# Performance work log

Hardware: AMD Instinct MI355X
Metric: run time of the kernel (lower is better)

## Reference

```python
import jax, jax.numpy as jnp
import numpy as np
from jax import lax
from jax.scipy.special import logsumexp

NUM_TAGS = 5
B, L = 16384, 512


def setup_inputs() -> dict:
    key = jax.random.key(0)
    k1, k2, k3, k4, k5 = jax.random.split(key, 5)
    emissions = jax.random.normal(k1, (B, L, NUM_TAGS), dtype=jnp.float32)
    tags = jax.random.randint(k2, (B, L), 0, NUM_TAGS)
    mask = jnp.ones((B, L), dtype=bool)
    # learned CRF parameters, init U(-0.1, 0.1) as in reset_parameters
    transitions = jax.random.uniform(k3, (NUM_TAGS, NUM_TAGS), minval=-0.1, maxval=0.1, dtype=jnp.float32)
    start_transitions = jax.random.uniform(k4, (NUM_TAGS,), minval=-0.1, maxval=0.1, dtype=jnp.float32)
    end_transitions = jax.random.uniform(k5, (NUM_TAGS,), minval=-0.1, maxval=0.1, dtype=jnp.float32)
    return {
        "emissions": emissions,
        "transitions": transitions,
        "start_transitions": start_transitions,
        "end_transitions": end_transitions,
        "tags": tags,
        "mask": mask,
    }


def reference(emissions, transitions, start_transitions, end_transitions, tags, mask):
    """CRF mean negative log-likelihood: log_partition - gold_score (both batch means)."""
    Bs, Ls, C = emissions.shape
    maskf = mask.astype(emissions.dtype)

    # ---- log partition (forward algorithm); note: original torch code's
    # mask application here is a no-op (where(mask, s, s)), reproduced faithfully.
    init_score = start_transitions[None, :] + emissions[:, 0]  # (B, C)

    def step(score, em_i):
        # score: (B, C) over previous tag; em_i: (B, C)
        nxt = logsumexp(score[:, :, None] + transitions[None, :, :] + em_i[:, None, :], axis=1)
        return nxt, None

    ems = jnp.swapaxes(emissions[:, 1:], 0, 1)  # (L-1, B, C)
    final_score, _ = lax.scan(step, init_score, ems)
    log_den = logsumexp(final_score + end_transitions[None, :], axis=1).mean()

    # ---- gold path score (fully vectorized over time)
    s0 = start_transitions[tags[:, 0]] + jnp.take_along_axis(emissions[:, 0], tags[:, :1], axis=1)[:, 0]
    trans_scores = transitions[tags[:, :-1], tags[:, 1:]]  # (B, L-1)
    em_at_tags = jnp.take_along_axis(emissions, tags[:, :, None], axis=2)[:, :, 0]  # (B, L)
    path_score = s0 + ((trans_scores + em_at_tags[:, 1:]) * maskf[:, 1:]).sum(axis=1)
    last_idx = mask.sum(axis=1).astype(jnp.int32) - 1  # (B,)
    last_tags = jnp.take_along_axis(tags, last_idx[:, None], axis=1)[:, 0]
    log_num = (path_score + end_transitions[last_tags]).mean()

    return log_den - log_num
```

## Files before the change

kernel.cpp:

```cpp
#include <hip/hip_runtime.h>

#define NTAGS 5
#define BATCH 16384
#define SEQL 512
#define TT 4
#define RECF 32

__device__ __forceinline__ float f4c(float4 v, int c) {
    switch (c & 3) { case 0: return v.x; case 1: return v.y; case 2: return v.z; default: return v.w; }
}
__device__ __forceinline__ int i4c(int4 v, int c) {
    switch (c & 3) { case 0: return v.x; case 1: return v.y; case 2: return v.z; default: return v.w; }
}
__device__ __forceinline__ float sel5v(float a0, float a1, float a2, float a3, float a4, int t) {
    float r = a0;
    r = (t == 1) ? a1 : r;
    r = (t == 2) ? a2 : r;
    r = (t == 3) ? a3 : r;
    r = (t == 4) ? a4 : r;
    return r;
}
__device__ __forceinline__ float rfl(float x) {
    return __int_as_float(__builtin_amdgcn_readfirstlane(__float_as_int(x)));
}

struct P1State {
    float M[25];
    float logS;
    float path;
    int prev;
};

__device__ __forceinline__ void p1_tile(const float4 tb[5], const int4 tg, bool sk0,
                                        P1State& st, const float eT[25],
                                        const float* ldsT, const float stR[5]) {
#pragma unroll
    for (int t = 0; t < TT; ++t) {
#define EMX(j) f4c(tb[(t * 5 + (j)) >> 2], (t * 5 + (j)) & 3)
        const float e0 = EMX(0), e1 = EMX(1), e2 = EMX(2), e3 = EMX(3), e4 = EMX(4);
#undef EMX
        const int tag = i4c(tg, t);
        const float emtag = sel5v(e0, e1, e2, e3, e4, tag);
        if (sk0 && t == 0) {
            st.path += sel5v(stR[0], stR[1], stR[2], stR[3], stR[4], tag) + emtag;
        } else {
            const float ex0 = __expf(e0), ex1 = __expf(e1), ex2 = __expf(e2),
                        ex3 = __expf(e3), ex4 = __expf(e4);
#pragma unroll
            for (int i = 0; i < 5; ++i) {
                const float m0 = st.M[i * 5 + 0], m1 = st.M[i * 5 + 1], m2 = st.M[i * 5 + 2],
                            m3 = st.M[i * 5 + 3], m4 = st.M[i * 5 + 4];
#pragma unroll
                for (int j = 0; j < 5; ++j) {
                    float a = m0 * eT[j];
                    a = fmaf(m1, eT[5 + j], a);
                    a = fmaf(m2, eT[10 + j], a);
                    a = fmaf(m3, eT[15 + j], a);
                    a = fmaf(m4, eT[20 + j], a);
                    const float exj = (j == 0) ? ex0 : (j == 1) ? ex1 : (j == 2) ? ex2
                                     : (j == 3) ? ex3 : ex4;
                    st.M[i * 5 + j] = a * exj;
                }
            }
            st.path += ldsT[st.prev * 5 + tag] + emtag;
        }
        st.prev = tag;
    }
    float m = st.M[0];
#pragma unroll
    for (int i = 1; i < 25; ++i) m = fmaxf(m, st.M[i]);
    st.logS += __logf(m);
    const float rc = __builtin_amdgcn_rcpf(m);
#pragma unroll
    for (int i = 0; i < 25; ++i) st.M[i] *= rc;
}

template <int NCHUNK>
__global__ __launch_bounds__(256) void crf_phase1(
    const float* __restrict__ emis, const float* __restrict__ trans,
    const float* __restrict__ startT, const int* __restrict__ tags,
    float* __restrict__ ws) {
    constexpr int CHUNKL = SEQL / NCHUNK;
    constexpr int NTILE = CHUNKL / TT;
    __shared__ float ldsT[25];
    const int tid = threadIdx.x;
    if (tid < 25) ldsT[tid] = trans[tid];
    __syncthreads();

    float eT[25];
#pragma unroll
    for (int i = 0; i < 25; ++i) eT[i] = rfl(__expf(trans[i]));
    float stR[5];
#pragma unroll
    for (int j = 0; j < 5; ++j) stR[j] = rfl(startT[j]);

    const int gt = blockIdx.x * 256 + tid;
    const int seq = gt / NCHUNK;
    const int chunk = gt & (NCHUNK - 1);
    const bool first = (chunk == 0);

    const float4* esrc =
        (const float4*)(emis + (size_t)seq * (SEQL * NTAGS) + chunk * (CHUNKL * NTAGS));
    const int tbase = seq * SEQL + chunk * CHUNKL;
    const int4* tsrc = (const int4*)(tags + tbase);

    P1State st;
#pragma unroll
    for (int i = 0; i < 25; ++i) st.M[i] = 0.f;
    st.M[0] = st.M[6] = st.M[12] = st.M[18] = st.M[24] = 1.f;
    st.logS = 0.f;
    st.path = 0.f;
    st.prev = first ? 0 : tags[tbase - 1];

#pragma unroll 1
    for (int tp = 0; tp < NTILE; ++tp) {
        float4 tb[5];
#pragma unroll
        for (int k = 0; k < 5; ++k) tb[k] = esrc[tp * 5 + k];
        const int4 tg = tsrc[tp];
        p1_tile(tb, tg, first && (tp == 0), st, eT, ldsT, stR);
    }

    float4* rec = (float4*)(ws + (size_t)gt * RECF);
#pragma unroll
    for (int k = 0; k < 6; ++k)
        rec[k] = make_float4(st.M[4 * k], st.M[4 * k + 1], st.M[4 * k + 2], st.M[4 * k + 3]);
    rec[6] = make_float4(st.M[24], st.logS, st.path, 0.f);
}

__device__ __forceinline__ void p2_combine(const float4 r[7], float v[5], float& logZ,
                                           float& path) {
#define MM(i, j) f4c(r[((i) * 5 + (j)) >> 2], ((i) * 5 + (j)) & 3)
    float nv[5];
#pragma unroll
    for (int j = 0; j < 5; ++j) {
        float a = v[0] * MM(0, j);
        a = fmaf(v[1], MM(1, j), a);
        a = fmaf(v[2], MM(2, j), a);
        a = fmaf(v[3], MM(3, j), a);
        a = fmaf(v[4], MM(4, j), a);
        nv[j] = a;
    }
#undef MM
    logZ += r[6].y;
    path += r[6].z;
    const float m = fmaxf(fmaxf(fmaxf(nv[0], nv[1]), fmaxf(nv[2], nv[3])), nv[4]);
    logZ += __logf(m);
    const float rc = __builtin_amdgcn_rcpf(m);
#pragma unroll
    for (int j = 0; j < 5; ++j) v[j] = nv[j] * rc;
}

template <int NCHUNK>
__global__ __launch_bounds__(64) void crf_phase2(
    const float* __restrict__ emis, const float* __restrict__ startT,
    const float* __restrict__ endT, const int* __restrict__ tags,
    const float* __restrict__ ws, float* __restrict__ out) {
    const int seq = blockIdx.x * 64 + threadIdx.x;
    const float* eb = emis + (size_t)seq * (SEQL * NTAGS);
    const float4 e03 = *(const float4*)eb;
    const float e4v = eb[4];
    const float s0 = startT[0] + e03.x, s1 = startT[1] + e03.y, s2 = startT[2] + e03.z,
                s3 = startT[3] + e03.w, s4 = startT[4] + e4v;
    const float m0 = fmaxf(fmaxf(fmaxf(s0, s1), fmaxf(s2, s3)), s4);
    float v[5] = {__expf(s0 - m0), __expf(s1 - m0), __expf(s2 - m0), __expf(s3 - m0),
                  __expf(s4 - m0)};
    float logZ = m0, path = 0.f;

    const float4* wsb = (const float4*)(ws + (size_t)seq * NCHUNK * RECF);
    float4 rA[7], rB[7];
#pragma unroll
    for (int k = 0; k < 7; ++k) rA[k] = wsb[k];

#pragma unroll 1
    for (int c = 0; c < NCHUNK; c += 2) {
#pragma unroll
        for (int k = 0; k < 7; ++k) rB[k] = wsb[(c + 1) * 8 + k];
        p2_combine(rA, v, logZ, path);
        const int nx = (c + 2 < NCHUNK) ? c + 2 : c;
#pragma unroll
        for (int k = 0; k < 7; ++k) rA[k] = wsb[nx * 8 + k];
        p2_combine(rB, v, logZ, path);
    }

    const float en0 = endT[0], en1 = endT[1], en2 = endT[2], en3 = endT[3], en4 = endT[4];
    float sden = v[0] * __expf(en0);
    sden = fmaf(v[1], __expf(en1), sden);
    sden = fmaf(v[2], __expf(en2), sden);
    sden = fmaf(v[3], __expf(en3), sden);
    sden = fmaf(v[4], __expf(en4), sden);
    const float den = logZ + __logf(sden);

    const int lastTag = tags[seq * SEQL + (SEQL - 1)];
    const float num = path + sel5v(en0, en1, en2, en3, en4, lastTag);

    float val = (den - num) * (1.0f / (float)BATCH);
#pragma unroll
    for (int off = 32; off > 0; off >>= 1) val += __shfl_xor(val, off, 64);
    if (threadIdx.x == 0) atomicAdd(out, val);
}

extern "C" void kernel_launch(void* const* d_in, const int* in_sizes, int n_in,
                              void* d_out, int out_size, void* d_ws, size_t ws_size,
                              hipStream_t stream) {
    const float* emis = (const float*)d_in[0];
    const float* trans = (const float*)d_in[1];
    const float* startT = (const float*)d_in[2];
    const float* endT = (const float*)d_in[3];
    const int* tags = (const int*)d_in[4];
    float* out = (float*)d_out;
    float* ws = (float*)d_ws;

    hipMemsetAsync(out, 0, sizeof(float), stream);
    const size_t need16 = (size_t)BATCH * 16 * RECF * sizeof(float);
    if (ws_size >= need16) {
        crf_phase1<16><<<dim3(BATCH * 16 / 256), dim3(256), 0, stream>>>(emis, trans,
                                                                         startT, tags, ws);
        crf_phase2<16><<<dim3(BATCH / 64), dim3(64), 0, stream>>>(emis, startT, endT,
                                                                  tags, ws, out);
    } else {
        crf_phase1<8><<<dim3(BATCH * 8 / 256), dim3(256), 0, stream>>>(emis, trans,
                                                                       startT, tags, ws);
        crf_phase2<8><<<dim3(BATCH / 64), dim3(64), 0, stream>>>(emis, startT, endT,
                                                                 tags, ws, out);
    }
}
```

Measured before the change: 329.4 us.

## Stage emissions through LDS as bf16, use 32 chunks, pack bf16 chunk records

Phase 1 now uses 64-thread blocks that cooperatively load a contiguous emission and tag slab with coalesced float4 loads. The data goes into LDS, emissions as bf16 pairs and tags as bytes. Each thread then processes a 16-step chunk (32 chunks per sequence) with renormalization every 8 steps. Chunk matrices are written as bf16 in a transposed, batch-major layout so phase 2 reads them coalesced with half the bytes. This targets global-load inefficiency and workspace traffic, but rounding emissions and the transfer matrices to bf16 changes the numerics relative to fp32.

```diff
diff --git a/kernel.cpp b/kernel.cpp
--- a/kernel.cpp
+++ b/kernel.cpp
@@ -3,15 +3,11 @@
 #define NTAGS 5
 #define BATCH 16384
 #define SEQL 512
-#define TT 4
-#define RECF 32
-
-__device__ __forceinline__ float f4c(float4 v, int c) {
-    switch (c & 3) { case 0: return v.x; case 1: return v.y; case 2: return v.z; default: return v.w; }
-}
-__device__ __forceinline__ int i4c(int4 v, int c) {
-    switch (c & 3) { case 0: return v.x; case 1: return v.y; case 2: return v.z; default: return v.w; }
-}
+#define NCHUNK 32
+#define CHUNKL 16
+#define EW 41
+#define TW 5
+
 __device__ __forceinline__ float sel5v(float a0, float a1, float a2, float a3, float a4, int t) {
     float r = a0;
     r = (t == 1) ? a1 : r;
@@ -23,68 +19,45 @@
 __device__ __forceinline__ float rfl(float x) {
     return __int_as_float(__builtin_amdgcn_readfirstlane(__float_as_int(x)));
 }
-
-struct P1State {
-    float M[25];
-    float logS;
-    float path;
-    int prev;
-};
-
-__device__ __forceinline__ void p1_tile(const float4 tb[5], const int4 tg, bool sk0,
-                                        P1State& st, const float eT[25],
-                                        const float* ldsT, const float stR[5]) {
-#pragma unroll
-    for (int t = 0; t < TT; ++t) {
-#define EMX(j) f4c(tb[(t * 5 + (j)) >> 2], (t * 5 + (j)) & 3)
-        const float e0 = EMX(0), e1 = EMX(1), e2 = EMX(2), e3 = EMX(3), e4 = EMX(4);
-#undef EMX
-        const int tag = i4c(tg, t);
-        const float emtag = sel5v(e0, e1, e2, e3, e4, tag);
-        if (sk0 && t == 0) {
-            st.path += sel5v(stR[0], stR[1], stR[2], stR[3], stR[4], tag) + emtag;
-        } else {
-            const float ex0 = __expf(e0), ex1 = __expf(e1), ex2 = __expf(e2),
-                        ex3 = __expf(e3), ex4 = __expf(e4);
-#pragma unroll
-            for (int i = 0; i < 5; ++i) {
-                const float m0 = st.M[i * 5 + 0], m1 = st.M[i * 5 + 1], m2 = st.M[i * 5 + 2],
-                            m3 = st.M[i * 5 + 3], m4 = st.M[i * 5 + 4];
-#pragma unroll
-                for (int j = 0; j < 5; ++j) {
-                    float a = m0 * eT[j];
-                    a = fmaf(m1, eT[5 + j], a);
-                    a = fmaf(m2, eT[10 + j], a);
-                    a = fmaf(m3, eT[15 + j], a);
-                    a = fmaf(m4, eT[20 + j], a);
-                    const float exj = (j == 0) ? ex0 : (j == 1) ? ex1 : (j == 2) ? ex2
-                                     : (j == 3) ? ex3 : ex4;
-                    st.M[i * 5 + j] = a * exj;
-                }
-            }
-            st.path += ldsT[st.prev * 5 + tag] + emtag;
-        }
-        st.prev = tag;
-    }
-    float m = st.M[0];
-#pragma unroll
-    for (int i = 1; i < 25; ++i) m = fmaxf(m, st.M[i]);
-    st.logS += __logf(m);
-    const float rc = __builtin_amdgcn_rcpf(m);
-#pragma unroll
-    for (int i = 0; i < 25; ++i) st.M[i] *= rc;
-}
-
-template <int NCHUNK>
-__global__ __launch_bounds__(256) void crf_phase1(
+__device__ __forceinline__ unsigned bf16rne(float x) {
+    const unsigned b = __float_as_uint(x);
+    return (b + 0x7FFFu + ((b >> 16) & 1u)) >> 16;
+}
+__device__ __forceinline__ float bflo(unsigned w) { return __uint_as_float(w << 16); }
+__device__ __forceinline__ float bfhi(unsigned w) { return __uint_as_float(w & 0xFFFF0000u); }
+
+__global__ __launch_bounds__(64) void crf_phase1(
     const float* __restrict__ emis, const float* __restrict__ trans,
     const float* __restrict__ startT, const int* __restrict__ tags,
-    float* __restrict__ ws) {
-    constexpr int CHUNKL = SEQL / NCHUNK;
-    constexpr int NTILE = CHUNKL / TT;
+    int4* __restrict__ ws) {
+    __shared__ unsigned eLds[64 * EW];
+    __shared__ unsigned tagLds[64 * TW];
     __shared__ float ldsT[25];
+
     const int tid = threadIdx.x;
+    const int gt0 = blockIdx.x * 64;
     if (tid < 25) ldsT[tid] = trans[tid];
+
+    const float4* esrc4 = (const float4*)emis + (size_t)gt0 * 20;
+#pragma unroll
+    for (int i = 0; i < 20; ++i) {
+        const float4 v = esrc4[i * 64 + tid];
+        const int f = i * 256 + tid * 4;
+        const int tau = f / 80;
+        const int h = f - tau * 80;
+        eLds[tau * EW + (h >> 1)] = bf16rne(v.x) | (bf16rne(v.y) << 16);
+        eLds[tau * EW + (h >> 1) + 1] = bf16rne(v.z) | (bf16rne(v.w) << 16);
+    }
+    const int4* tsrc4 = (const int4*)tags + (size_t)gt0 * 4;
+#pragma unroll
+    for (int i = 0; i < 4; ++i) {
+        const int4 tv = tsrc4[i * 64 + tid];
+        const int g = i * 256 + tid * 4;
+        const int tau = g >> 4;
+        const int k = (g & 15) >> 2;
+        tagLds[tau * TW + k] = (unsigned)tv.x | ((unsigned)tv.y << 8) |
+                               ((unsigned)tv.z << 16) | ((unsigned)tv.w << 24);
+    }
     __syncthreads();
 
     float eT[25];
@@ -94,56 +67,113 @@
 #pragma unroll
     for (int j = 0; j < 5; ++j) stR[j] = rfl(startT[j]);
 
-    const int gt = blockIdx.x * 256 + tid;
-    const int seq = gt / NCHUNK;
-    const int chunk = gt & (NCHUNK - 1);
-    const bool first = (chunk == 0);
-
-    const float4* esrc =
-        (const float4*)(emis + (size_t)seq * (SEQL * NTAGS) + chunk * (CHUNKL * NTAGS));
-    const int tbase = seq * SEQL + chunk * CHUNKL;
-    const int4* tsrc = (const int4*)(tags + tbase);
-
-    P1State st;
-#pragma unroll
-    for (int i = 0; i < 25; ++i) st.M[i] = 0.f;
-    st.M[0] = st.M[6] = st.M[12] = st.M[18] = st.M[24] = 1.f;
-    st.logS = 0.f;
-    st.path = 0.f;
-    st.prev = first ? 0 : tags[tbase - 1];
-
-#pragma unroll 1
-    for (int tp = 0; tp < NTILE; ++tp) {
-        float4 tb[5];
-#pragma unroll
-        for (int k = 0; k < 5; ++k) tb[k] = esrc[tp * 5 + k];
-        const int4 tg = tsrc[tp];
-        p1_tile(tb, tg, first && (tp == 0), st, eT, ldsT, stR);
-    }
-
-    float4* rec = (float4*)(ws + (size_t)gt * RECF);
-#pragma unroll
-    for (int k = 0; k < 6; ++k)
-        rec[k] = make_float4(st.M[4 * k], st.M[4 * k + 1], st.M[4 * k + 2], st.M[4 * k + 3]);
-    rec[6] = make_float4(st.M[24], st.logS, st.path, 0.f);
-}
-
-__device__ __forceinline__ void p2_combine(const float4 r[7], float v[5], float& logZ,
+    float M[25];
+#pragma unroll
+    for (int i = 0; i < 25; ++i) M[i] = 0.f;
+    M[0] = M[6] = M[12] = M[18] = M[24] = 1.f;
+    float logS = 0.f, path = 0.f;
+    const bool first = (tid & 31) == 0;
+    int prev = first ? 0 : (int)(tagLds[(tid - 1) * TW + 3] >> 24);
+
+    const unsigned* eb = &eLds[tid * EW];
+    const unsigned* tb = &tagLds[tid * TW];
+
+#pragma unroll 2
+    for (int sp = 0; sp < 8; ++sp) {
+        const unsigned w0 = eb[sp * 5 + 0], w1 = eb[sp * 5 + 1], w2 = eb[sp * 5 + 2],
+                       w3 = eb[sp * 5 + 3], w4 = eb[sp * 5 + 4];
+        const unsigned twrd = tb[sp >> 1];
+#pragma unroll
+        for (int half = 0; half < 2; ++half) {
+            const int s = sp * 2 + half;
+            const float e0 = half ? bfhi(w2) : bflo(w0);
+            const float e1 = half ? bflo(w3) : bfhi(w0);
+            const float e2 = half ? bfhi(w3) : bflo(w1);
+            const float e3 = half ? bflo(w4) : bfhi(w1);
+            const float e4 = half ? bfhi(w4) : bflo(w2);
+            const int tag = (int)((twrd >> ((s & 3) * 8)) & 255u);
+            const float emtag = sel5v(e0, e1, e2, e3, e4, tag);
+            if (first && s == 0) {
+                path += sel5v(stR[0], stR[1], stR[2], stR[3], stR[4], tag) + emtag;
+            } else {
+                const float ex0 = __expf(e0), ex1 = __expf(e1), ex2 = __expf(e2),
+                            ex3 = __expf(e3), ex4 = __expf(e4);
+#pragma unroll
+                for (int i = 0; i < 5; ++i) {
+                    const float m0 = M[i * 5 + 0], m1 = M[i * 5 + 1], m2 = M[i * 5 + 2],
+                                m3 = M[i * 5 + 3], m4 = M[i * 5 + 4];
+#pragma unroll
+                    for (int j = 0; j < 5; ++j) {
+                        float a = m0 * eT[j];
+                        a = fmaf(m1, eT[5 + j], a);
+                        a = fmaf(m2, eT[10 + j], a);
+                        a = fmaf(m3, eT[15 + j], a);
+                        a = fmaf(m4, eT[20 + j], a);
+                        const float exj = (j == 0) ? ex0 : (j == 1) ? ex1 : (j == 2) ? ex2
+                                         : (j == 3) ? ex3 : ex4;
+                        M[i * 5 + j] = a * exj;
+                    }
+                }
+                path += ldsT[prev * 5 + tag] + emtag;
+            }
+            prev = tag;
+        }
+        if ((sp & 3) == 3) {
+            float m = M[0];
+#pragma unroll
+            for (int i = 1; i < 25; ++i) m = fmaxf(m, M[i]);
+            logS += __logf(m);
+            const float rc = __builtin_amdgcn_rcpf(m);
+#pragma unroll
+            for (int i = 0; i < 25; ++i) M[i] *= rc;
+        }
+    }
+
+    unsigned rw[16];
+#pragma unroll
+    for (int j = 0; j < 12; ++j) rw[j] = bf16rne(M[2 * j]) | (bf16rne(M[2 * j + 1]) << 16);
+    rw[12] = bf16rne(M[24]);
+    rw[13] = __float_as_uint(logS);
+    rw[14] = __float_as_uint(path);
+    rw[15] = 0u;
+    const int gt = gt0 + tid;
+    const int seq = gt >> 5, chunk = gt & 31;
+#pragma unroll
+    for (int k = 0; k < 4; ++k)
+        ws[(size_t)(chunk * 4 + k) * BATCH + seq] =
+            make_int4((int)rw[4 * k], (int)rw[4 * k + 1], (int)rw[4 * k + 2],
+                      (int)rw[4 * k + 3]);
+}
+
+__device__ __forceinline__ void p2_combine(const int4 r[4], float v[5], float& logZ,
                                            float& path) {
-#define MM(i, j) f4c(r[((i) * 5 + (j)) >> 2], ((i) * 5 + (j)) & 3)
+    unsigned w[16];
+#pragma unroll
+    for (int k = 0; k < 4; ++k) {
+        w[4 * k + 0] = (unsigned)r[k].x;
+        w[4 * k + 1] = (unsigned)r[k].y;
+        w[4 * k + 2] = (unsigned)r[k].z;
+        w[4 * k + 3] = (unsigned)r[k].w;
+    }
+    float M[25];
+#pragma unroll
+    for (int j = 0; j < 12; ++j) {
+        M[2 * j] = bflo(w[j]);
+        M[2 * j + 1] = bfhi(w[j]);
+    }
+    M[24] = bflo(w[12]);
     float nv[5];
 #pragma unroll
     for (int j = 0; j < 5; ++j) {
-        float a = v[0] * MM(0, j);
-        a = fmaf(v[1], MM(1, j), a);
-        a = fmaf(v[2], MM(2, j), a);
-        a = fmaf(v[3], MM(3, j), a);
-        a = fmaf(v[4], MM(4, j), a);
+        float a = v[0] * M[j];
+        a = fmaf(v[1], M[5 + j], a);
+        a = fmaf(v[2], M[10 + j], a);
+        a = fmaf(v[3], M[15 + j], a);
+        a = fmaf(v[4], M[20 + j], a);
         nv[j] = a;
     }
-#undef MM
-    logZ += r[6].y;
-    path += r[6].z;
+    logZ += __uint_as_float(w[13]);
+    path += __uint_as_float(w[14]);
     const float m = fmaxf(fmaxf(fmaxf(nv[0], nv[1]), fmaxf(nv[2], nv[3])), nv[4]);
     logZ += __logf(m);
     const float rc = __builtin_amdgcn_rcpf(m);
@@ -151,15 +181,14 @@
     for (int j = 0; j < 5; ++j) v[j] = nv[j] * rc;
 }
 
-template <int NCHUNK>
 __global__ __launch_bounds__(64) void crf_phase2(
     const float* __restrict__ emis, const float* __restrict__ startT,
     const float* __restrict__ endT, const int* __restrict__ tags,
-    const float* __restrict__ ws, float* __restrict__ out) {
+    const int4* __restrict__ ws, float* __restrict__ out) {
     const int seq = blockIdx.x * 64 + threadIdx.x;
-    const float* eb = emis + (size_t)seq * (SEQL * NTAGS);
-    const float4 e03 = *(const float4*)eb;
-    const float e4v = eb[4];
+    const float* ebp = emis + (size_t)seq * (SEQL * NTAGS);
+    const float4 e03 = *(const float4*)ebp;
+    const float e4v = ebp[4];
     const float s0 = startT[0] + e03.x, s1 = startT[1] + e03.y, s2 = startT[2] + e03.z,
                 s3 = startT[3] + e03.w, s4 = startT[4] + e4v;
     const float m0 = fmaxf(fmaxf(fmaxf(s0, s1), fmaxf(s2, s3)), s4);
@@ -167,19 +196,18 @@
                   __expf(s4 - m0)};
     float logZ = m0, path = 0.f;
 
-    const float4* wsb = (const float4*)(ws + (size_t)seq * NCHUNK * RECF);
-    float4 rA[7], rB[7];
-#pragma unroll
-    for (int k = 0; k < 7; ++k) rA[k] = wsb[k];
+    int4 rA[4], rB[4];
+#pragma unroll
+    for (int k = 0; k < 4; ++k) rA[k] = ws[(size_t)k * BATCH + seq];
 
 #pragma unroll 1
     for (int c = 0; c < NCHUNK; c += 2) {
 #pragma unroll
-        for (int k = 0; k < 7; ++k) rB[k] = wsb[(c + 1) * 8 + k];
+        for (int k = 0; k < 4; ++k) rB[k] = ws[(size_t)((c + 1) * 4 + k) * BATCH + seq];
         p2_combine(rA, v, logZ, path);
         const int nx = (c + 2 < NCHUNK) ? c + 2 : c;
 #pragma unroll
-        for (int k = 0; k < 7; ++k) rA[k] = wsb[nx * 8 + k];
+        for (int k = 0; k < 4; ++k) rA[k] = ws[(size_t)(nx * 4 + k) * BATCH + seq];
         p2_combine(rB, v, logZ, path);
     }
 
@@ -209,19 +237,11 @@
     const float* endT = (const float*)d_in[3];
     const int* tags = (const int*)d_in[4];
     float* out = (float*)d_out;
-    float* ws = (float*)d_ws;
+    int4* ws = (int4*)d_ws;
 
     hipMemsetAsync(out, 0, sizeof(float), stream);
-    const size_t need16 = (size_t)BATCH * 16 * RECF * sizeof(float);
-    if (ws_size >= need16) {
-        crf_phase1<16><<<dim3(BATCH * 16 / 256), dim3(256), 0, stream>>>(emis, trans,
-                                                                         startT, tags, ws);
-        crf_phase2<16><<<dim3(BATCH / 64), dim3(64), 0, stream>>>(emis, startT, endT,
-                                                                  tags, ws, out);
-    } else {
-        crf_phase1<8><<<dim3(BATCH * 8 / 256), dim3(256), 0, stream>>>(emis, trans,
-                                                                       startT, tags, ws);
-        crf_phase2<8><<<dim3(BATCH / 64), dim3(64), 0, stream>>>(emis, startT, endT,
-                                                                 tags, ws, out);
-    }
-}
+    crf_phase1<<<dim3(BATCH * NCHUNK / 64), dim3(64), 0, stream>>>(emis, trans, startT,
+                                                                   tags, ws);
+    crf_phase2<<<dim3(BATCH / 64), dim3(64), 0, stream>>>(emis, startT, endT, tags, ws,
+                                                          out);
+}
```

After: 322.4 us. -2.1%, faster.
